# Kernel tuning notes

Measured on AMD Instinct MI355X. Metric: run time of the kernel, lower is better.

Reference implementation:

```python
import jax, jax.numpy as jnp
import numpy as np

HEADS = 8
HEAD_DIM = 64
DIM = HEADS * HEAD_DIM  # 512
D_IN = 256


def setup_inputs() -> dict:
    key = jax.random.key(0)
    ks = jax.random.split(key, 10)
    B, N, M, K = 4, 2048, 2048, 32
    x = jax.random.normal(ks[0], (B, N, D_IN), dtype=jnp.float32)
    context = jax.random.normal(ks[1], (B, M, D_IN), dtype=jnp.float32)
    index_pairs = jax.random.randint(ks[2], (B, N, K), 0, M, dtype=jnp.int32)
    mask_q = jnp.ones((B, N), dtype=bool)
    mask_k = jnp.ones((B, M), dtype=bool)
    s_in = 1.0 / np.sqrt(D_IN)
    s_dim = 1.0 / np.sqrt(DIM)
    Wq = jax.random.normal(ks[3], (D_IN, DIM), dtype=jnp.float32) * s_in
    bq = jnp.zeros((DIM,), dtype=jnp.float32)
    Wk = jax.random.normal(ks[4], (D_IN, DIM), dtype=jnp.float32) * s_in
    Wv = jax.random.normal(ks[5], (D_IN, DIM), dtype=jnp.float32) * s_in
    Wout = jax.random.normal(ks[6], (DIM, D_IN), dtype=jnp.float32) * s_dim
    bout = jnp.zeros((D_IN,), dtype=jnp.float32)
    return {"x": x, "context": context, "index_pairs": index_pairs,
            "mask_q": mask_q, "mask_k": mask_k,
            "Wq": Wq, "bq": bq, "Wk": Wk, "Wv": Wv, "Wout": Wout, "bout": bout}


def reference(x, context, index_pairs, mask_q, mask_k, Wq, bq, Wk, Wv, Wout, bout):
    h, d = HEADS, HEAD_DIM
    B, N, _ = x.shape
    K = index_pairs.shape[-1]
    q = x @ Wq + bq                       # [b, n, h*d]
    k = context @ Wk                      # [b, m, h*d]
    v = context @ Wv                      # [b, m, h*d]
    # Gather local neighborhoods: [b, n, K, h*d]
    k = jnp.take_along_axis(k[:, :, None, :], index_pairs[:, :, :, None], axis=1)
    v = jnp.take_along_axis(v[:, :, None, :], index_pairs[:, :, :, None], axis=1)
    k = k.reshape(B, N, K, h, d)
    v = v.reshape(B, N, K, h, d)
    q = q.reshape(B, N, h, d)
    sim = jnp.einsum('bihd,bikhd->bikh', q, k) * (d ** -0.5)  # [b, n, K, h]
    big_neg = jnp.finfo(jnp.float32).min
    sim = jnp.where(mask_q[:, :, None, None], sim, big_neg)
    mk = jnp.take_along_axis(mask_k[:, :, None], index_pairs, axis=1)  # [b, n, K]
    sim = jnp.where(mk[:, :, :, None], sim, big_neg)
    attn = jax.nn.softmax(sim, axis=-2)   # softmax over K neighbors
    out = jnp.einsum('bikh,bikhd->bihd', attn, v)
    out = out.reshape(B, N, h * d)
    return out @ Wout + bout
```

## Files before the change

### kernel.cpp

```cpp
#include <hip/hip_runtime.h>
#include <hip/hip_bf16.h>

#define HEADS    8
#define HEAD_DIM 64
#define DIM      512
#define D_IN     256
#define BATCH    4
#define SEQ      2048
#define KNBR     32
#define ROWS     (BATCH*SEQ)
#define NQKV     (3*DIM)

typedef __hip_bfloat16 bf16;
typedef __attribute__((ext_vector_type(8))) short bf16x8;
typedef __attribute__((ext_vector_type(4))) float floatx4;

__device__ __forceinline__ ushort f2bf(float f) {
    union { bf16 h; ushort u; } c; c.h = __float2bfloat16(f); return c.u;
}

__device__ __forceinline__ void load_bf16x8(const bf16* p, float* o) {
    uint4 raw = *(const uint4*)p;
    unsigned u[4] = {raw.x, raw.y, raw.z, raw.w};
#pragma unroll
    for (int i = 0; i < 4; i++) {
        o[2*i]   = __uint_as_float(u[i] << 16);
        o[2*i+1] = __uint_as_float(u[i] & 0xffff0000u);
    }
}

__device__ __forceinline__ void async16(const bf16* g, bf16* l) {
    __builtin_amdgcn_global_load_lds(
        (const __attribute__((address_space(1))) void*)g,
        (__attribute__((address_space(3))) void*)l, 16, 0, 0);
}

__global__ __launch_bounds__(256)
void prep_kernel(const float* __restrict__ x, const float* __restrict__ ctx,
                 const float* __restrict__ Wq, const float* __restrict__ Wk,
                 const float* __restrict__ Wv, const float* __restrict__ Wo,
                 const float* __restrict__ bq,
                 bf16* __restrict__ xb, bf16* __restrict__ cb,
                 bf16* __restrict__ Wqkv, bf16* __restrict__ WoT,
                 float* __restrict__ biasq)
{
    const int b = blockIdx.x;
    if (b < 2048) {
        const int gid  = b * 256 + threadIdx.x;
        const int half = (ROWS * D_IN) / 8;
        const float* src; bf16* dst; int f;
        if (gid < half) { src = x;   dst = xb; f = gid * 8; }
        else            { src = ctx; dst = cb; f = (gid - half) * 8; }
        float4 v0 = *(const float4*)(src + f);
        float4 v1 = *(const float4*)(src + f + 4);
        uint4 o;
        o.x = f2bf(v0.x) | ((unsigned)f2bf(v0.y) << 16);
        o.y = f2bf(v0.z) | ((unsigned)f2bf(v0.w) << 16);
        o.z = f2bf(v1.x) | ((unsigned)f2bf(v1.y) << 16);
        o.w = f2bf(v1.z) | ((unsigned)f2bf(v1.w) << 16);
        *(uint4*)(dst + f) = o;
        return;
    }
    int p = b - 2048;
    if (p >= 512) {
        int i = (p - 512) * 256 + threadIdx.x;
        if (i < NQKV) biasq[i] = (i < DIM) ? bq[i] : 0.f;
        return;
    }
    __shared__ float tile[32][33];
    int z, tb;
    if (p < 384) { z = p >> 7; tb = p & 127; }
    else         { z = 3;      tb = p - 384; }
    const float* src; bf16* dst; int C, bx, by;
    if      (z == 0) { src = Wq; dst = Wqkv;              C = 512; }
    else if (z == 1) { src = Wk; dst = Wqkv + 512 * 256;  C = 512; }
    else if (z == 2) { src = Wv; dst = Wqkv + 1024 * 256; C = 512; }
    else             { src = Wo; dst = WoT;               C = 256; }
    if (z < 3) { bx = tb & 15; by = tb >> 4; }
    else       { bx = tb & 7;  by = tb >> 3; }
    const int r0 = by * 32, c0 = bx * 32;
    const int tx = threadIdx.x & 31, ty = threadIdx.x >> 5;
#pragma unroll
    for (int i = 0; i < 4; i++)
        tile[ty + 8*i][tx] = src[(size_t)(r0 + ty + 8*i) * C + c0 + tx];
    __syncthreads();
#pragma unroll
    for (int i = 0; i < 4; i++)
        dst[(size_t)(c0 + ty + 8*i) * ((z < 3) ? 256 : 512) + r0 + tx] =
            __float2bfloat16(tile[tx][ty + 8*i]);
}

template<int TM, int TN, int KD, int NN, int CBF16>
__global__ __launch_bounds__(256)
void mfma_gemm(const bf16* __restrict__ A, const bf16* __restrict__ A2, int split,
               const bf16* __restrict__ B, const float* __restrict__ bias,
               void* __restrict__ C)
{
    constexpr int MI = TM / 32, NI = TN / 32;
    constexpr int NT = KD / 64;
    static_assert((TM * 64 + TN * 64) * 2 * 2 <= 65536, "LDS budget");
    __shared__ bf16 As[2][TM * 64];
    __shared__ bf16 Bs[2][TN * 64];
    const int t    = threadIdx.x;
    const int lane = t & 63;
    const int w    = t >> 6;
    const int row0 = blockIdx.y * TM;
    const int col0 = blockIdx.x * TN;
    const bf16* Au = (col0 < split) ? A : A2;
    const int wm   = (w >> 1) * (TM / 2);
    const int wn   = (w & 1) * (TN / 2);

    const int sr = t >> 3;
    const int sc = (t & 7) * 8;

    floatx4 acc[MI][NI];
#pragma unroll
    for (int i = 0; i < MI; i++)
#pragma unroll
        for (int j = 0; j < NI; j++) acc[i][j] = (floatx4){0.f, 0.f, 0.f, 0.f};

    const int fr = lane & 15;
    const int fq = lane >> 4;

    auto stage = [&](int buf, int k0) {
#pragma unroll
        for (int is = 0; is < TM / 32; is++)
            async16(Au + (size_t)(row0 + is*32 + sr) * KD + k0 + sc,
                    &As[buf][is*2048 + w*512]);
#pragma unroll
        for (int is = 0; is < TN / 32; is++)
            async16(B + (size_t)(col0 + is*32 + sr) * KD + k0 + sc,
                    &Bs[buf][is*2048 + w*512]);
    };

    stage(0, 0);
    __syncthreads();

#pragma unroll
    for (int tt = 0; tt < NT; ++tt) {
        const int cur = tt & 1;
        if (tt + 1 < NT) stage(cur ^ 1, (tt + 1) * 64);
#pragma unroll
        for (int ks = 0; ks < 2; ks++) {
            bf16x8 af[MI], bfr[NI];
#pragma unroll
            for (int mi = 0; mi < MI; mi++)
                af[mi] = *(const bf16x8*)&As[cur][(wm + mi*16 + fr) * 64 + ks*32 + fq*8];
#pragma unroll
            for (int ni = 0; ni < NI; ni++)
                bfr[ni] = *(const bf16x8*)&Bs[cur][(wn + ni*16 + fr) * 64 + ks*32 + fq*8];
#pragma unroll
            for (int mi = 0; mi < MI; mi++)
#pragma unroll
                for (int ni = 0; ni < NI; ni++)
                    acc[mi][ni] = __builtin_amdgcn_mfma_f32_16x16x32_bf16(
                        af[mi], bfr[ni], acc[mi][ni], 0, 0, 0);
        }
        __syncthreads();
    }

    constexpr int WN  = NI * 16;
    constexpr int STR = WN + 4;
    float* wep = (float*)As + w * (16 * STR);

#pragma unroll
    for (int mi = 0; mi < MI; mi++) {
#pragma unroll
        for (int ni = 0; ni < NI; ni++) {
            const float bv = bias[col0 + wn + ni*16 + fr];
#pragma unroll
            for (int r = 0; r < 4; r++)
                wep[(fq*4 + r) * STR + ni*16 + fr] = acc[mi][ni][r] + bv;
        }
        if constexpr (CBF16) {
            constexpr int LPR = WN / 8;
            constexpr int RPP = 64 / LPR;
            constexpr int NP  = 16 / RPP;
#pragma unroll
            for (int p = 0; p < NP; p++) {
                const int rl = p * RPP + lane / LPR;
                const int cl = (lane % LPR) * 8;
                const float4 a  = *(const float4*)&wep[rl * STR + cl];
                const float4 b2 = *(const float4*)&wep[rl * STR + cl + 4];
                uint4 o;
                o.x = f2bf(a.x)  | ((unsigned)f2bf(a.y)  << 16);
                o.y = f2bf(a.z)  | ((unsigned)f2bf(a.w)  << 16);
                o.z = f2bf(b2.x) | ((unsigned)f2bf(b2.y) << 16);
                o.w = f2bf(b2.z) | ((unsigned)f2bf(b2.w) << 16);
                *(uint4*)((bf16*)C + (size_t)(row0 + wm + mi*16 + rl) * NN
                                   + col0 + wn + cl) = o;
            }
        } else {
            constexpr int LPR = WN / 4;
            constexpr int RPP = 64 / LPR;
            constexpr int NP  = 16 / RPP;
#pragma unroll
            for (int p = 0; p < NP; p++) {
                const int rl = p * RPP + lane / LPR;
                const int cl = (lane % LPR) * 4;
                const float4 a = *(const float4*)&wep[rl * STR + cl];
                *(float4*)((float*)C + (size_t)(row0 + wm + mi*16 + rl) * NN
                                     + col0 + wn + cl) = a;
            }
        }
    }
}

__global__ __launch_bounds__(256, 4)
void attn_kernel(const bf16* __restrict__ qkv, const int* __restrict__ idx,
                 bf16* __restrict__ att)
{
    __shared__ int   s_off[4][KNBR];
    __shared__ float s_part[4][16][68];
    __shared__ float s_aw[4][KNBR][HEADS];

    const int t    = threadIdx.x;
    const int w    = t >> 6;
    const int lane = t & 63;
    const int i    = blockIdx.x;
    const int batch  = (i >> 1) & 3;
    const int within = ((i >> 3) << 1) | (i & 1);
    const int bn     = batch * SEQ + within * 4 + w;

    int* woff = s_off[w];
    float (*wpart)[68] = s_part[w];
    float* waw = &s_aw[w][0][0];

    if (lane < KNBR) woff[lane] = idx[(size_t)bn * KNBR + lane] * (NQKV * 2);

    float qr[8];
    load_bf16x8(qkv + (size_t)bn * NQKV + lane * 8, qr);

    const char* kbase = (const char*)qkv +
        ((size_t)batch * SEQ * NQKV + DIM) * 2 + lane * 16;
    const int h = lane >> 3;

    float sim[4];
#pragma unroll
    for (int pass = 0; pass < 2; pass++) {
#pragma unroll 8
        for (int kk = 0; kk < 16; kk++) {
            const int off = woff[pass * 16 + kk];
            float k8[8];
            load_bf16x8((const bf16*)(kbase + off), k8);
            float d = 0.f;
#pragma unroll
            for (int e = 0; e < 8; e++) d += qr[e] * k8[e];
            wpart[kk][lane] = d;
        }
#pragma unroll
        for (int r = 0; r < 2; r++) {
            const int p = lane + 64 * r;
            const float4* pp = (const float4*)&wpart[p >> 3][(p & 7) * 8];
            float4 a = pp[0], b2 = pp[1];
            sim[pass*2 + r] = (a.x + a.y + a.z + a.w + b2.x + b2.y + b2.z + b2.w) * 0.125f;
        }
    }

    float mx = fmaxf(fmaxf(sim[0], sim[1]), fmaxf(sim[2], sim[3]));
    mx = fmaxf(mx, __shfl_xor(mx, 8));
    mx = fmaxf(mx, __shfl_xor(mx, 16));
    mx = fmaxf(mx, __shfl_xor(mx, 32));
    float e4[4], ss = 0.f;
#pragma unroll
    for (int r = 0; r < 4; r++) { e4[r] = __expf(sim[r] - mx); ss += e4[r]; }
    ss += __shfl_xor(ss, 8);
    ss += __shfl_xor(ss, 16);
    ss += __shfl_xor(ss, 32);
    const float inv = 1.f / ss;
    const int kk0 = lane >> 3, hh = lane & 7;
#pragma unroll
    for (int r = 0; r < 4; r++) waw[(kk0 + 8*r) * HEADS + hh] = e4[r] * inv;

    float acc[8] = {};
#pragma unroll 8
    for (int kk = 0; kk < KNBR; kk++) {
        const int off = woff[kk];
        const float a = waw[kk * HEADS + h];
        float v8[8];
        load_bf16x8((const bf16*)(kbase + off + DIM * 2), v8);
#pragma unroll
        for (int e = 0; e < 8; e++) acc[e] += a * v8[e];
    }

    uint4 o;
    o.x = f2bf(acc[0]) | ((unsigned)f2bf(acc[1]) << 16);
    o.y = f2bf(acc[2]) | ((unsigned)f2bf(acc[3]) << 16);
    o.z = f2bf(acc[4]) | ((unsigned)f2bf(acc[5]) << 16);
    o.w = f2bf(acc[6]) | ((unsigned)f2bf(acc[7]) << 16);
    *(uint4*)(att + (size_t)bn * DIM + lane * 8) = o;
}

extern "C" void kernel_launch(void* const* d_in, const int* in_sizes, int n_in,
                              void* d_out, int out_size, void* d_ws, size_t ws_size,
                              hipStream_t stream)
{
    const float* x    = (const float*)d_in[0];
    const float* ctx  = (const float*)d_in[1];
    const int*   idx  = (const int*)d_in[2];
    const float* Wq   = (const float*)d_in[5];
    const float* bq   = (const float*)d_in[6];
    const float* Wk   = (const float*)d_in[7];
    const float* Wv   = (const float*)d_in[8];
    const float* Wout = (const float*)d_in[9];
    const float* bout = (const float*)d_in[10];

    char*  ws    = (char*)d_ws;
    bf16*  xb    = (bf16*)(ws);
    bf16*  cb    = (bf16*)(ws + (size_t) 4*1024*1024);
    bf16*  Wqkv  = (bf16*)(ws + (size_t) 8*1024*1024);
    bf16*  WoT   = (bf16*)(ws + (size_t) 9*1024*1024);
    float* biasq = (float*)(ws + (size_t) 9*1024*1024 + 524288);
    bf16*  Cqkv  = (bf16*)(ws + (size_t)10*1024*1024);
    bf16*  atb   = (bf16*)(ws + (size_t)34*1024*1024);

    prep_kernel<<<dim3(2048 + 512 + 6), dim3(256), 0, stream>>>(
        x, ctx, Wq, Wk, Wv, Wout, bq, xb, cb, Wqkv, WoT, biasq);
    mfma_gemm<128,128,256,1536,1><<<dim3(12, 64), dim3(256), 0, stream>>>(
        xb, cb, 512, Wqkv, biasq, Cqkv);
    attn_kernel<<<dim3(2048), dim3(256), 0, stream>>>(Cqkv, idx, atb);
    mfma_gemm<64,64,512,256,0><<<dim3(4, 128), dim3(256), 0, stream>>>(
        atb, atb, 1 << 30, WoT, bout, d_out);
}
```

Baseline: 145.0 us.

## Fuse neighborhood attention with output projection via in-block MFMA

Attention and the output projection now run in one kernel. Each 512-thread block processes 16 queries, keeps their attention outputs in LDS as bf16, and multiplies them by WoT using 16x16x32 bf16 MFMA before adding the bias and writing fp32 output. This removes the intermediate attention buffer round-trip and one kernel launch. In exchange each block reads all of WoT (256x512 bf16) straight from global memory, so the grid re-reads the weights about 512 times. The kernel also uses more LDS per block and launches fewer blocks.

```diff
diff --git a/kernel.cpp b/kernel.cpp
--- a/kernel.cpp
+++ b/kernel.cpp
@@ -98,7 +98,6 @@
 {
     constexpr int MI = TM / 32, NI = TN / 32;
     constexpr int NT = KD / 64;
-    static_assert((TM * 64 + TN * 64) * 2 * 2 <= 65536, "LDS budget");
     __shared__ bf16 As[2][TM * 64];
     __shared__ bf16 Bs[2][TN * 64];
     const int t    = threadIdx.x;
@@ -206,13 +205,16 @@
     }
 }
 
-__global__ __launch_bounds__(256, 4)
-void attn_kernel(const bf16* __restrict__ qkv, const int* __restrict__ idx,
-                 bf16* __restrict__ att)
+__global__ __launch_bounds__(512, 4)
+void attn_out_kernel(const bf16* __restrict__ qkv, const int* __restrict__ idx,
+                     const bf16* __restrict__ WoT, const float* __restrict__ bout,
+                     float* __restrict__ outp)
 {
-    __shared__ int   s_off[4][KNBR];
-    __shared__ float s_part[4][16][68];
-    __shared__ float s_aw[4][KNBR][HEADS];
+    __shared__ int   s_off[8][KNBR];
+    __shared__ float s_part[8][16][68];
+    __shared__ float s_aw[8][KNBR][HEADS];
+    __shared__ bf16  s_att[16][520];
+    __shared__ float s_out[16][260];
 
     const int t    = threadIdx.x;
     const int w    = t >> 6;
@@ -220,75 +222,112 @@
     const int i    = blockIdx.x;
     const int batch  = (i >> 1) & 3;
     const int within = ((i >> 3) << 1) | (i & 1);
-    const int bn     = batch * SEQ + within * 4 + w;
+    const int q0     = batch * SEQ + within * 16;
 
     int* woff = s_off[w];
     float (*wpart)[68] = s_part[w];
     float* waw = &s_aw[w][0][0];
 
-    if (lane < KNBR) woff[lane] = idx[(size_t)bn * KNBR + lane] * (NQKV * 2);
-
-    float qr[8];
-    load_bf16x8(qkv + (size_t)bn * NQKV + lane * 8, qr);
-
     const char* kbase = (const char*)qkv +
         ((size_t)batch * SEQ * NQKV + DIM) * 2 + lane * 16;
     const int h = lane >> 3;
 
-    float sim[4];
-#pragma unroll
-    for (int pass = 0; pass < 2; pass++) {
+#pragma unroll
+    for (int sub = 0; sub < 2; sub++) {
+        const int qloc = w * 2 + sub;
+        const int q    = q0 + qloc;
+
+        if (lane < KNBR) woff[lane] = idx[(size_t)q * KNBR + lane] * (NQKV * 2);
+
+        float qr[8];
+        load_bf16x8(qkv + (size_t)q * NQKV + lane * 8, qr);
+
+        float sim[4];
+#pragma unroll
+        for (int pass = 0; pass < 2; pass++) {
 #pragma unroll 8
-        for (int kk = 0; kk < 16; kk++) {
-            const int off = woff[pass * 16 + kk];
-            float k8[8];
-            load_bf16x8((const bf16*)(kbase + off), k8);
-            float d = 0.f;
-#pragma unroll
-            for (int e = 0; e < 8; e++) d += qr[e] * k8[e];
-            wpart[kk][lane] = d;
-        }
-#pragma unroll
-        for (int r = 0; r < 2; r++) {
-            const int p = lane + 64 * r;
-            const float4* pp = (const float4*)&wpart[p >> 3][(p & 7) * 8];
-            float4 a = pp[0], b2 = pp[1];
-            sim[pass*2 + r] = (a.x + a.y + a.z + a.w + b2.x + b2.y + b2.z + b2.w) * 0.125f;
-        }
-    }
-
-    float mx = fmaxf(fmaxf(sim[0], sim[1]), fmaxf(sim[2], sim[3]));
-    mx = fmaxf(mx, __shfl_xor(mx, 8));
-    mx = fmaxf(mx, __shfl_xor(mx, 16));
-    mx = fmaxf(mx, __shfl_xor(mx, 32));
-    float e4[4], ss = 0.f;
-#pragma unroll
-    for (int r = 0; r < 4; r++) { e4[r] = __expf(sim[r] - mx); ss += e4[r]; }
-    ss += __shfl_xor(ss, 8);
-    ss += __shfl_xor(ss, 16);
-    ss += __shfl_xor(ss, 32);
-    const float inv = 1.f / ss;
-    const int kk0 = lane >> 3, hh = lane & 7;
-#pragma unroll
-    for (int r = 0; r < 4; r++) waw[(kk0 + 8*r) * HEADS + hh] = e4[r] * inv;
-
-    float acc[8] = {};
+            for (int kk = 0; kk < 16; kk++) {
+                const int off = woff[pass * 16 + kk];
+                float k8[8];
+                load_bf16x8((const bf16*)(kbase + off), k8);
+                float d = 0.f;
+#pragma unroll
+                for (int e = 0; e < 8; e++) d += qr[e] * k8[e];
+                wpart[kk][lane] = d;
+            }
+#pragma unroll
+            for (int r = 0; r < 2; r++) {
+                const int p = lane + 64 * r;
+                const float4* pp = (const float4*)&wpart[p >> 3][(p & 7) * 8];
+                float4 a = pp[0], b2 = pp[1];
+                sim[pass*2 + r] = (a.x + a.y + a.z + a.w + b2.x + b2.y + b2.z + b2.w) * 0.125f;
+            }
+        }
+
+        float mx = fmaxf(fmaxf(sim[0], sim[1]), fmaxf(sim[2], sim[3]));
+        mx = fmaxf(mx, __shfl_xor(mx, 8));
+        mx = fmaxf(mx, __shfl_xor(mx, 16));
+        mx = fmaxf(mx, __shfl_xor(mx, 32));
+        float e4[4], ss = 0.f;
+#pragma unroll
+        for (int r = 0; r < 4; r++) { e4[r] = __expf(sim[r] - mx); ss += e4[r]; }
+        ss += __shfl_xor(ss, 8);
+        ss += __shfl_xor(ss, 16);
+        ss += __shfl_xor(ss, 32);
+        const float inv = 1.f / ss;
+        const int kk0 = lane >> 3, hh = lane & 7;
+#pragma unroll
+        for (int r = 0; r < 4; r++) waw[(kk0 + 8*r) * HEADS + hh] = e4[r] * inv;
+
+        float acc[8] = {};
 #pragma unroll 8
-    for (int kk = 0; kk < KNBR; kk++) {
-        const int off = woff[kk];
-        const float a = waw[kk * HEADS + h];
-        float v8[8];
-        load_bf16x8((const bf16*)(kbase + off + DIM * 2), v8);
-#pragma unroll
-        for (int e = 0; e < 8; e++) acc[e] += a * v8[e];
-    }
-
-    uint4 o;
-    o.x = f2bf(acc[0]) | ((unsigned)f2bf(acc[1]) << 16);
-    o.y = f2bf(acc[2]) | ((unsigned)f2bf(acc[3]) << 16);
-    o.z = f2bf(acc[4]) | ((unsigned)f2bf(acc[5]) << 16);
-    o.w = f2bf(acc[6]) | ((unsigned)f2bf(acc[7]) << 16);
-    *(uint4*)(att + (size_t)bn * DIM + lane * 8) = o;
+        for (int kk = 0; kk < KNBR; kk++) {
+            const int off = woff[kk];
+            const float a = waw[kk * HEADS + h];
+            float v8[8];
+            load_bf16x8((const bf16*)(kbase + off + DIM * 2), v8);
+#pragma unroll
+            for (int e = 0; e < 8; e++) acc[e] += a * v8[e];
+        }
+
+        uint4 o;
+        o.x = f2bf(acc[0]) | ((unsigned)f2bf(acc[1]) << 16);
+        o.y = f2bf(acc[2]) | ((unsigned)f2bf(acc[3]) << 16);
+        o.z = f2bf(acc[4]) | ((unsigned)f2bf(acc[5]) << 16);
+        o.w = f2bf(acc[6]) | ((unsigned)f2bf(acc[7]) << 16);
+        *(uint4*)&s_att[qloc][lane * 8] = o;
+    }
+    __syncthreads();
+
+    const int fr = lane & 15, fq = lane >> 4;
+    const int wn = w * 32;
+    floatx4 o0 = (floatx4){0.f,0.f,0.f,0.f};
+    floatx4 o1 = (floatx4){0.f,0.f,0.f,0.f};
+#pragma unroll
+    for (int ks = 0; ks < 16; ks++) {
+        bf16x8 af = *(const bf16x8*)&s_att[fr][ks*32 + fq*8];
+        bf16x8 b0 = *(const bf16x8*)&WoT[(size_t)(wn      + fr) * DIM + ks*32 + fq*8];
+        bf16x8 b1 = *(const bf16x8*)&WoT[(size_t)(wn + 16 + fr) * DIM + ks*32 + fq*8];
+        o0 = __builtin_amdgcn_mfma_f32_16x16x32_bf16(af, b0, o0, 0, 0, 0);
+        o1 = __builtin_amdgcn_mfma_f32_16x16x32_bf16(af, b1, o1, 0, 0, 0);
+    }
+#pragma unroll
+    for (int r = 0; r < 4; r++) {
+        s_out[fq*4 + r][wn      + fr] = o0[r];
+        s_out[fq*4 + r][wn + 16 + fr] = o1[r];
+    }
+    __syncthreads();
+
+    const int row = t >> 5;
+    const int col = (t & 31) * 8;
+    float4 a  = *(const float4*)&s_out[row][col];
+    float4 b2 = *(const float4*)&s_out[row][col + 4];
+    const float4 ba = *(const float4*)&bout[col];
+    const float4 bb = *(const float4*)&bout[col + 4];
+    a.x += ba.x; a.y += ba.y; a.z += ba.z; a.w += ba.w;
+    b2.x += bb.x; b2.y += bb.y; b2.z += bb.z; b2.w += bb.w;
+    *(float4*)(outp + (size_t)(q0 + row) * D_IN + col)     = a;
+    *(float4*)(outp + (size_t)(q0 + row) * D_IN + col + 4) = b2;
 }
 
 extern "C" void kernel_launch(void* const* d_in, const int* in_sizes, int n_in,
@@ -312,13 +351,11 @@
     bf16*  WoT   = (bf16*)(ws + (size_t) 9*1024*1024);
     float* biasq = (float*)(ws + (size_t) 9*1024*1024 + 524288);
     bf16*  Cqkv  = (bf16*)(ws + (size_t)10*1024*1024);
-    bf16*  atb   = (bf16*)(ws + (size_t)34*1024*1024);
 
     prep_kernel<<<dim3(2048 + 512 + 6), dim3(256), 0, stream>>>(
         x, ctx, Wq, Wk, Wv, Wout, bq, xb, cb, Wqkv, WoT, biasq);
     mfma_gemm<128,128,256,1536,1><<<dim3(12, 64), dim3(256), 0, stream>>>(
         xb, cb, 512, Wqkv, biasq, Cqkv);
-    attn_kernel<<<dim3(2048), dim3(256), 0, stream>>>(Cqkv, idx, atb);
-    mfma_gemm<64,64,512,256,0><<<dim3(4, 128), dim3(256), 0, stream>>>(
-        atb, atb, 1 << 30, WoT, bout, d_out);
-}
+    attn_out_kernel<<<dim3(512), dim3(512), 0, stream>>>(
+        Cqkv, idx, WoT, bout, (float*)d_out);
+}
```

New measurement: 144.0 us (median of 2 runs). About the same (-0.7%).
